# Kernel optimization log

Hardware: AMD Instinct MI355X
Metric: run time of the kernel (lower is better)

The kernel has to match this reference:

```python
import jax, jax.numpy as jnp
import numpy as np

B, TED, G, N, E, MD, NOISE = 10000, 512, 64, 2000, 64000, 15, 128
PAC = 10
PACDIM = (TED + NOISE) * PAC  # 6400
D0, D1 = 1024, 512


def _linear_params(k, fan_in, fan_out):
    kw, kb = jax.random.split(k)
    lim = 1.0 / np.sqrt(fan_in)
    w = jax.random.uniform(kw, (fan_in, fan_out), minval=-lim, maxval=lim, dtype=jnp.float32)
    b = jax.random.uniform(kb, (fan_out,), minval=-lim, maxval=lim, dtype=jnp.float32)
    return w, b


def setup_inputs() -> dict:
    key = jax.random.key(0)
    ks = jax.random.split(key, 12)
    inp = {
        'input_': jax.random.normal(ks[0], (B, TED), dtype=jnp.float32),
        'graphs_x': jax.random.normal(ks[1], (G, N, 1), dtype=jnp.float32),
        'edge_index': jax.random.randint(ks[2], (G, 2, E), 0, N, dtype=jnp.int32),
        'graph_ids': jax.random.randint(ks[3], (B,), 0, G, dtype=jnp.int32),
        'chain': jax.random.normal(ks[4], (B, 1), dtype=jnp.float32),
        'metadata': jax.random.normal(ks[5], (B, MD), dtype=jnp.float32),
    }
    inp['gcn_w'], inp['gcn_b'] = _linear_params(ks[6], 1, 1)
    inp['meta_w'], inp['meta_b'] = _linear_params(ks[7], 1 + MD, 32)
    inp['gme_w'], inp['gme_b'] = _linear_params(ks[8], N + 32, NOISE)
    inp['seq_w0'], inp['seq_b0'] = _linear_params(ks[9], PACDIM, D0)
    inp['seq_w1'], inp['seq_b1'] = _linear_params(ks[10], D0, D1)
    inp['seq_w2'], inp['seq_b2'] = _linear_params(ks[11], D1, 1)
    return inp


def _gcn_one(x, ei, gcn_w, gcn_b):
    # GCNConv(1,1) with self-loops and symmetric normalization.
    loops = jnp.arange(N, dtype=ei.dtype)
    src = jnp.concatenate([ei[0], loops])
    dst = jnp.concatenate([ei[1], loops])
    deg = jax.ops.segment_sum(jnp.ones_like(src, dtype=x.dtype), dst, num_segments=N)
    dinv = jax.lax.rsqrt(deg)  # deg >= 1 due to self-loops
    norm = dinv[src] * dinv[dst]  # [E+N]
    xw = x @ gcn_w  # [N,1]
    msg = xw[src] * norm[:, None]
    out = jax.ops.segment_sum(msg, dst, num_segments=N) + gcn_b
    return out.reshape(-1)  # flatten -> [N]


def reference(input_, graphs_x, edge_index, graph_ids, chain, metadata,
              gcn_w, gcn_b, meta_w, meta_b, gme_w, gme_b,
              seq_w0, seq_b0, seq_w1, seq_b1, seq_w2, seq_b2):
    # per-unique-graph GCN, vectorized over G graphs
    gcn_out = jax.vmap(lambda x, ei: _gcn_one(x, ei, gcn_w, gcn_b))(graphs_x, edge_index)  # [G,N]
    graph_emb = gcn_out[graph_ids]  # gather: [B,N]
    all_meta = jnp.concatenate([chain, metadata], axis=1)  # [B,1+MD]
    meta_emb = jax.nn.relu(all_meta @ meta_w + meta_b)  # [B,32]
    noise = jnp.concatenate([graph_emb, meta_emb], axis=1) @ gme_w + gme_b  # [B,NOISE]
    h = jnp.concatenate([input_, noise], axis=1).reshape(-1, PACDIM)  # [B/PAC, PACDIM]
    h = jax.nn.leaky_relu(h @ seq_w0 + seq_b0, 0.2)  # dropout omitted (eval mode)
    h = jax.nn.leaky_relu(h @ seq_w1 + seq_b1, 0.2)
    return h @ seq_w2 + seq_b2  # [B/PAC, 1]
```

## Files before the change

### kernel.cpp

```cpp
#include <hip/hip_runtime.h>

typedef __bf16 bf16_t;
typedef __bf16 bf16x4 __attribute__((ext_vector_type(4)));
typedef __bf16 bf16x8 __attribute__((ext_vector_type(8)));
typedef float floatx4 __attribute__((ext_vector_type(4)));

#define G_GRAPHS 64
#define N_NODES 2000
#define N_EDGES 64000
#define BATCH 10000
#define TED_ 512
#define NOISE_ 128
#define PACDIM_ 6400
#define D0_ 1024
#define D1_ 512
#define MROWS 1000
#define ESPLIT 8
#define EPB (N_EDGES / ESPLIT)
#define S0 8
#define S1 8

__device__ __forceinline__ void glds16(const void* g, void* l) {
    __builtin_amdgcn_global_load_lds(
        (__attribute__((address_space(1))) void*)(g),
        (__attribute__((address_space(3))) void*)(l), 16, 0, 0);
}

__global__ __launch_bounds__(256) void prep_kernel(
    const int* __restrict__ edge_index, float* __restrict__ degs_part,
    const float* __restrict__ in, bf16_t* __restrict__ A,
    const float* __restrict__ W0, bf16_t* __restrict__ W0t,
    const float* __restrict__ W1, bf16_t* __restrict__ W1t)
{
    __shared__ float h[N_NODES];
    __shared__ float t[32][33];
    const int b = blockIdx.x, tid = threadIdx.x;
    if (b < 512) {
        const int s = b & 7, g = b >> 3;
        for (int n = tid; n < N_NODES; n += 256) h[n] = 0.f;
        __syncthreads();
        const int* dst = edge_index + (size_t)g * 2 * N_EDGES + N_EDGES + s * EPB;
        for (int e = tid; e < EPB; e += 256) atomicAdd(&h[dst[e]], 1.0f);
        __syncthreads();
        float* dp = degs_part + ((size_t)g * ESPLIT + s) * N_NODES;
        for (int n = tid; n < N_NODES; n += 256) dp[n] = h[n];
        return;
    }
    if (b < 5512) {
        int idx = (b - 512) * 256 + tid;
        float4 v = ((const float4*)in)[idx];
        int bb = idx >> 7;
        int c = (idx & 127) << 2;
        int r = bb / 10, slot = bb - r * 10;
        bf16x4 o = { (bf16_t)v.x, (bf16_t)v.y, (bf16_t)v.z, (bf16_t)v.w };
        *(bf16x4*)(A + (size_t)r * PACDIM_ + slot * 640 + c) = o;
        return;
    }
    const float* W; bf16_t* Wt; int Rr, Cc, c0, r0;
    if (b < 11912) {
        int tile = b - 5512;
        W = W0; Wt = W0t; Rr = PACDIM_; Cc = D0_;
        c0 = (tile & 31) << 5; r0 = (tile >> 5) << 5;
    } else {
        int tile = b - 11912;
        W = W1; Wt = W1t; Rr = D0_; Cc = D1_;
        c0 = (tile & 15) << 5; r0 = (tile >> 4) << 5;
    }
    int tx = tid & 31, ty = tid >> 5;
    for (int yy = ty; yy < 32; yy += 8)
        t[yy][tx] = W[(size_t)(r0 + yy) * Cc + c0 + tx];
    __syncthreads();
    for (int yy = ty; yy < 32; yy += 8)
        Wt[(size_t)(c0 + yy) * Rr + r0 + tx] = (bf16_t)t[tx][yy];
}

__global__ __launch_bounds__(512) void msg_kernel(
    const float* __restrict__ graphs_x, const int* __restrict__ edge_index,
    const float* __restrict__ degs_part, float* __restrict__ outs_part)
{
    __shared__ float xs[N_NODES];
    __shared__ float dv[N_NODES];
    __shared__ float oh[N_NODES];
    const int g = blockIdx.y, s = blockIdx.x, tid = threadIdx.x;
    const float* xg = graphs_x + (size_t)g * N_NODES;
    const float* dgp = degs_part + (size_t)g * ESPLIT * N_NODES;
    for (int n = tid; n < N_NODES; n += 512) {
        xs[n] = xg[n];
        float d = 1.0f;
        for (int p = 0; p < ESPLIT; p++) d += dgp[(size_t)p * N_NODES + n];
        dv[n] = rsqrtf(d);
        oh[n] = 0.f;
    }
    __syncthreads();
    const int* src = edge_index + (size_t)g * 2 * N_EDGES + s * EPB;
    const int* dst = src + N_EDGES;
    for (int e = tid; e < EPB; e += 512) {
        int ss = src[e], dd = dst[e];
        atomicAdd(&oh[dd], xs[ss] * dv[ss] * dv[dd]);
    }
    __syncthreads();
    float* op = outs_part + ((size_t)g * ESPLIT + s) * N_NODES;
    for (int n = tid; n < N_NODES; n += 512) op[n] = oh[n];
}

__global__ __launch_bounds__(512) void gnoise_kernel(
    const float* __restrict__ graphs_x, const float* __restrict__ degs_part,
    const float* __restrict__ outs_part,
    const float* __restrict__ gcn_w, const float* __restrict__ gcn_b,
    const float* __restrict__ gme_w, float* __restrict__ gnoise_p)
{
    __shared__ float of[500];
    __shared__ float part[4][128];
    const int s = blockIdx.x, g = blockIdx.y, tid = threadIdx.x;
    const int nBase = s * 500;
    const float w = gcn_w[0], bb = gcn_b[0];
    const float* dgp = degs_part + (size_t)g * ESPLIT * N_NODES;
    const float* otp = outs_part + (size_t)g * ESPLIT * N_NODES;
    for (int n = tid; n < 500; n += 512) {
        int gn = nBase + n;
        float d = 1.0f, o = 0.f;
        for (int p = 0; p < ESPLIT; p++) {
            d += dgp[(size_t)p * N_NODES + gn];
            o += otp[(size_t)p * N_NODES + gn];
        }
        of[n] = w * (o + graphs_x[(size_t)g * N_NODES + gn] / d) + bb;
    }
    __syncthreads();
    const int j = tid & 127, ch = tid >> 7;
    float acc = 0.f;
    const int n0 = ch * 125;
    for (int n = n0; n < n0 + 125; n++)
        acc += of[n] * gme_w[(size_t)(nBase + n) * 128 + j];
    part[ch][j] = acc;
    __syncthreads();
    if (tid < 128)
        gnoise_p[((size_t)g * 4 + s) * 128 + tid] =
            part[0][tid] + part[1][tid] + part[2][tid] + part[3][tid];
}

__global__ __launch_bounds__(256) void meta_kernel(
    const float* __restrict__ chain, const float* __restrict__ metadata,
    const int* __restrict__ graph_ids,
    const float* __restrict__ meta_w, const float* __restrict__ meta_b,
    const float* __restrict__ gme_w, const float* __restrict__ gme_b,
    const float* __restrict__ gnoise_p, bf16_t* __restrict__ A)
{
    int wid = (blockIdx.x * 256 + threadIdx.x) >> 6;
    int lane = threadIdx.x & 63;
    if (wid >= BATCH) return;
    const int b = wid;
    float me = 0.f;
    if (lane < 32) {
        me = meta_b[lane] + chain[b] * meta_w[lane];
        for (int i = 1; i < 16; i++)
            me += metadata[(size_t)b * 15 + (i - 1)] * meta_w[(size_t)i * 32 + lane];
        me = me > 0.f ? me : 0.f;
    }
    const int gid = graph_ids[b];
    const float* gp = gnoise_p + (size_t)gid * 4 * 128;
    const int j1 = lane, j2 = lane + 64;
    float n1 = gme_b[j1] + gp[j1] + gp[128 + j1] + gp[256 + j1] + gp[384 + j1];
    float n2 = gme_b[j2] + gp[j2] + gp[128 + j2] + gp[256 + j2] + gp[384 + j2];
    for (int k = 0; k < 32; k++) {
        float mk = __shfl(me, k, 64);
        const float* wrow = gme_w + (size_t)(N_NODES + k) * 128;
        n1 += mk * wrow[j1];
        n2 += mk * wrow[j2];
    }
    int r = b / 10, slot = b - r * 10;
    bf16_t* dp = A + (size_t)r * PACDIM_ + slot * 640 + TED_;
    dp[j1] = (bf16_t)n1;
    dp[j2] = (bf16_t)n2;
}

__global__ __launch_bounds__(256) void gemm_bt_splitk_kernel(
    const bf16_t* __restrict__ A,
    const bf16_t* __restrict__ Bt,
    float* __restrict__ P,
    int M, int N, int K, int KS, int zbits, int xbits, int Mp)
{
    __shared__ __align__(16) bf16_t As[2][128 * 32];
    __shared__ __align__(16) bf16_t Bs[2][128 * 32];
    const int tid = threadIdx.x;
    const int wave = tid >> 6;
    const int lane = tid & 63;
    const int id = blockIdx.x;
    const int z = id & ((1 << zbits) - 1);
    const int xt = (id >> zbits) & ((1 << xbits) - 1);
    const int yt = id >> (zbits + xbits);
    const int mBase = yt * 128;
    const int nBase = xt * 128;
    const int wm = (wave & 1) * 64;
    const int wn = (wave >> 1) * 64;

    floatx4 acc[4][4] = {};

    const int rA0 = tid >> 2, k80 = (tid & 3) * 8;
    int gm0 = mBase + rA0;      if (gm0 > M - 1) gm0 = M - 1;
    int gm1 = mBase + 64 + rA0; if (gm1 > M - 1) gm1 = M - 1;
    const bf16_t* aP0 = A + (size_t)gm0 * K + k80;
    const bf16_t* aP1 = A + (size_t)gm1 * K + k80;
    const bf16_t* bP0 = Bt + (size_t)(nBase + rA0) * K + k80;
    const bf16_t* bP1 = Bt + (size_t)(nBase + 64 + rA0) * K + k80;

    const int kq = (lane >> 4) * 8;
    const int mr = lane & 15;
    int aOff[4], bOff[4];
    for (int i = 0; i < 4; i++) aOff[i] = (wm + i * 16 + mr) * 32 + kq;
    for (int j = 0; j < 4; j++) bOff[j] = (wn + j * 16 + mr) * 32 + kq;

    const int nIter = KS >> 5;
    const int kc = z * KS;
    {
        char* lA = (char*)(&As[0][0]) + wave * 1024;
        char* lB = (char*)(&Bs[0][0]) + wave * 1024;
        glds16(aP0 + kc, lA);
        glds16(aP1 + kc, lA + 4096);
        glds16(bP0 + kc, lB);
        glds16(bP1 + kc, lB + 4096);
    }
    __syncthreads();
    for (int t = 0; t < nIter; ++t) {
        const int cur = t & 1;
        if (t + 1 < nIter) {
            const int kn = kc + (t + 1) * 32;
            char* lA = (char*)(&As[cur ^ 1][0]) + wave * 1024;
            char* lB = (char*)(&Bs[cur ^ 1][0]) + wave * 1024;
            glds16(aP0 + kn, lA);
            glds16(aP1 + kn, lA + 4096);
            glds16(bP0 + kn, lB);
            glds16(bP1 + kn, lB + 4096);
        }
        const bf16_t* aB = &As[cur][0];
        const bf16_t* bB = &Bs[cur][0];
        bf16x8 af[4], bfr[4];
        for (int i = 0; i < 4; i++) af[i] = *(const bf16x8*)(aB + aOff[i]);
        for (int j = 0; j < 4; j++) bfr[j] = *(const bf16x8*)(bB + bOff[j]);
        for (int i = 0; i < 4; i++)
            for (int j = 0; j < 4; j++)
                acc[i][j] = __builtin_amdgcn_mfma_f32_16x16x32_bf16(
                    af[i], bfr[j], acc[i][j], 0, 0, 0);
        __syncthreads();
    }

    float* Pz = P + (size_t)z * Mp * N;
    const int rq = (lane >> 4) * 4;
    const int cn = lane & 15;
    for (int j = 0; j < 4; j++) {
        int col = nBase + wn + j * 16 + cn;
        for (int i = 0; i < 4; i++)
            for (int r = 0; r < 4; r++) {
                int rowm = mBase + wm + i * 16 + rq + r;
                Pz[(size_t)rowm * N + col] = acc[i][j][r];
            }
    }
}

__global__ __launch_bounds__(256) void reduce_bias_leaky_kernel(
    const float* __restrict__ P, const float* __restrict__ bias,
    bf16_t* __restrict__ C, int M, int N, int Mp, int S)
{
    int idx = blockIdx.x * 256 + threadIdx.x;
    int total = M * (N >> 2);
    if (idx >= total) return;
    int nv = N >> 2;
    int r = idx / nv, c4 = (idx - r * nv) << 2;
    size_t off = (size_t)r * N + c4;
    size_t stride = (size_t)Mp * N;
    float4 v = *(const float4*)(P + off);
    for (int s = 1; s < S; s++) {
        float4 u = *(const float4*)(P + s * stride + off);
        v.x += u.x; v.y += u.y; v.z += u.z; v.w += u.w;
    }
    const float4 bv = *(const float4*)(bias + c4);
    v.x += bv.x; v.y += bv.y; v.z += bv.z; v.w += bv.w;
    v.x = v.x > 0.f ? v.x : 0.2f * v.x;
    v.y = v.y > 0.f ? v.y : 0.2f * v.y;
    v.z = v.z > 0.f ? v.z : 0.2f * v.z;
    v.w = v.w > 0.f ? v.w : 0.2f * v.w;
    bf16x4 o = { (bf16_t)v.x, (bf16_t)v.y, (bf16_t)v.z, (bf16_t)v.w };
    *(bf16x4*)(C + off) = o;
}

__global__ __launch_bounds__(256) void final_fused_kernel(
    const float* __restrict__ P, const float* __restrict__ b1,
    const float* __restrict__ w2, const float* __restrict__ b2,
    float* __restrict__ out, int Mp, int S)
{
    int wid = (blockIdx.x * 256 + threadIdx.x) >> 6;
    int lane = threadIdx.x & 63;
    if (wid >= MROWS) return;
    size_t stride = (size_t)Mp * D1_;
    const float* base = P + (size_t)wid * D1_;
    float s = 0.f;
    for (int i = 0; i < 8; i++) {
        int c = i * 64 + lane;
        float v = base[c];
        for (int z = 1; z < S; z++) v += base[(size_t)z * stride + c];
        v += b1[c];
        v = v > 0.f ? v : 0.2f * v;
        s += v * w2[c];
    }
    for (int off = 32; off; off >>= 1) s += __shfl_down(s, off, 64);
    if (lane == 0) out[wid] = s + b2[0];
}

extern "C" void kernel_launch(void* const* d_in, const int* in_sizes, int n_in,
                              void* d_out, int out_size, void* d_ws, size_t ws_size,
                              hipStream_t stream)
{
    const float* input_    = (const float*)d_in[0];
    const float* graphs_x  = (const float*)d_in[1];
    const int*   edge_idx  = (const int*)  d_in[2];
    const int*   graph_ids = (const int*)  d_in[3];
    const float* chain     = (const float*)d_in[4];
    const float* metadata  = (const float*)d_in[5];
    const float* gcn_w     = (const float*)d_in[6];
    const float* gcn_b     = (const float*)d_in[7];
    const float* meta_w    = (const float*)d_in[8];
    const float* meta_b    = (const float*)d_in[9];
    const float* gme_w     = (const float*)d_in[10];
    const float* gme_b     = (const float*)d_in[11];
    const float* seq_w0    = (const float*)d_in[12];
    const float* seq_b0    = (const float*)d_in[13];
    const float* seq_w1    = (const float*)d_in[14];
    const float* seq_b1    = (const float*)d_in[15];
    const float* seq_w2    = (const float*)d_in[16];
    const float* seq_b2    = (const float*)d_in[17];
    float* out = (float*)d_out;

    char* ws = (char*)d_ws;
    float*  degs_part = (float*)(ws + 0);
    float*  outs_part = (float*)(ws + 4096000);
    float*  gnoise_p  = (float*)(ws + 8192000);
    bf16_t* Abuf      = (bf16_t*)(ws + 8323072);
    bf16_t* W0t       = (bf16_t*)(ws + 21123072);
    bf16_t* W1t       = (bf16_t*)(ws + 34230272);
    bf16_t* H1        = (bf16_t*)(ws + 35278848);
    float*  P         = (float*)(ws + 37326848);

    prep_kernel<<<12424, 256, 0, stream>>>(
        edge_idx, degs_part, input_, Abuf, seq_w0, W0t, seq_w1, W1t);
    msg_kernel<<<dim3(ESPLIT, G_GRAPHS), 512, 0, stream>>>(
        graphs_x, edge_idx, degs_part, outs_part);
    gnoise_kernel<<<dim3(4, G_GRAPHS), 512, 0, stream>>>(
        graphs_x, degs_part, outs_part, gcn_w, gcn_b, gme_w, gnoise_p);
    meta_kernel<<<2500, 256, 0, stream>>>(
        chain, metadata, graph_ids, meta_w, meta_b, gme_w, gme_b,
        gnoise_p, Abuf);

    gemm_bt_splitk_kernel<<<512, 256, 0, stream>>>(
        Abuf, W0t, P, MROWS, D0_, PACDIM_, PACDIM_ / S0, 3, 3, 1024);
    reduce_bias_leaky_kernel<<<(MROWS * D0_ / 4 + 255) / 256, 256, 0, stream>>>(
        P, seq_b0, H1, MROWS, D0_, 1024, S0);

    gemm_bt_splitk_kernel<<<256, 256, 0, stream>>>(
        H1, W1t, P, MROWS, D1_, D0_, D0_ / S1, 3, 2, 1024);
    final_fused_kernel<<<(MROWS * 64 + 255) / 256, 256, 0, stream>>>(
        P, seq_b1, seq_w2, seq_b2, out, 1024, S1);
}
```

Measured before the change: 265.6 us.

## Swizzle GEMM LDS layout, split message pass finer, vectorize edge loads

The GEMM tile loader and fragment reader now XOR-swizzle the 8-element k-groups by row, so LDS reads of the bf16 tiles hit fewer bank conflicts. The GCN message kernel splits edges 16 ways instead of 8 and precomputes x*dinv per node, dropping one multiply and one LDS read per edge. Degree and message edge loops use int4 and int2 vector loads. The workspace layout is shifted to hold the larger partial buffer, and gnoise now sums 16 message partials, which adds a little reduction work.

```diff
diff --git a/kernel.cpp b/kernel.cpp
--- a/kernel.cpp
+++ b/kernel.cpp
@@ -17,6 +17,8 @@
 #define MROWS 1000
 #define ESPLIT 8
 #define EPB (N_EDGES / ESPLIT)
+#define MSPLIT 16
+#define EPB_MSG (N_EDGES / MSPLIT)
 #define S0 8
 #define S1 8
 
@@ -39,8 +41,13 @@
         const int s = b & 7, g = b >> 3;
         for (int n = tid; n < N_NODES; n += 256) h[n] = 0.f;
         __syncthreads();
-        const int* dst = edge_index + (size_t)g * 2 * N_EDGES + N_EDGES + s * EPB;
-        for (int e = tid; e < EPB; e += 256) atomicAdd(&h[dst[e]], 1.0f);
+        const int4* d4 = (const int4*)(edge_index + (size_t)g * 2 * N_EDGES
+                                       + N_EDGES + s * EPB);
+        for (int e = tid; e < EPB / 4; e += 256) {
+            int4 v = d4[e];
+            atomicAdd(&h[v.x], 1.0f); atomicAdd(&h[v.y], 1.0f);
+            atomicAdd(&h[v.z], 1.0f); atomicAdd(&h[v.w], 1.0f);
+        }
         __syncthreads();
         float* dp = degs_part + ((size_t)g * ESPLIT + s) * N_NODES;
         for (int n = tid; n < N_NODES; n += 256) dp[n] = h[n];
@@ -78,28 +85,31 @@
     const float* __restrict__ graphs_x, const int* __restrict__ edge_index,
     const float* __restrict__ degs_part, float* __restrict__ outs_part)
 {
-    __shared__ float xs[N_NODES];
-    __shared__ float dv[N_NODES];
+    __shared__ float ys[N_NODES];
+    __shared__ float dvl[N_NODES];
     __shared__ float oh[N_NODES];
     const int g = blockIdx.y, s = blockIdx.x, tid = threadIdx.x;
     const float* xg = graphs_x + (size_t)g * N_NODES;
     const float* dgp = degs_part + (size_t)g * ESPLIT * N_NODES;
     for (int n = tid; n < N_NODES; n += 512) {
-        xs[n] = xg[n];
         float d = 1.0f;
         for (int p = 0; p < ESPLIT; p++) d += dgp[(size_t)p * N_NODES + n];
-        dv[n] = rsqrtf(d);
+        float dv = rsqrtf(d);
+        dvl[n] = dv;
+        ys[n] = xg[n] * dv;
         oh[n] = 0.f;
     }
     __syncthreads();
-    const int* src = edge_index + (size_t)g * 2 * N_EDGES + s * EPB;
-    const int* dst = src + N_EDGES;
-    for (int e = tid; e < EPB; e += 512) {
-        int ss = src[e], dd = dst[e];
-        atomicAdd(&oh[dd], xs[ss] * dv[ss] * dv[dd]);
-    }
-    __syncthreads();
-    float* op = outs_part + ((size_t)g * ESPLIT + s) * N_NODES;
+    const int* src = edge_index + (size_t)g * 2 * N_EDGES + s * EPB_MSG;
+    const int2* s2 = (const int2*)src;
+    const int2* d2 = (const int2*)(src + N_EDGES);
+    for (int e = tid; e < EPB_MSG / 2; e += 512) {
+        int2 sv = s2[e], dd = d2[e];
+        atomicAdd(&oh[dd.x], ys[sv.x] * dvl[dd.x]);
+        atomicAdd(&oh[dd.y], ys[sv.y] * dvl[dd.y]);
+    }
+    __syncthreads();
+    float* op = outs_part + ((size_t)g * MSPLIT + s) * N_NODES;
     for (int n = tid; n < N_NODES; n += 512) op[n] = oh[n];
 }
 
@@ -115,14 +125,12 @@
     const int nBase = s * 500;
     const float w = gcn_w[0], bb = gcn_b[0];
     const float* dgp = degs_part + (size_t)g * ESPLIT * N_NODES;
-    const float* otp = outs_part + (size_t)g * ESPLIT * N_NODES;
+    const float* otp = outs_part + (size_t)g * MSPLIT * N_NODES;
     for (int n = tid; n < 500; n += 512) {
         int gn = nBase + n;
         float d = 1.0f, o = 0.f;
-        for (int p = 0; p < ESPLIT; p++) {
-            d += dgp[(size_t)p * N_NODES + gn];
-            o += otp[(size_t)p * N_NODES + gn];
-        }
+        for (int p = 0; p < ESPLIT; p++) d += dgp[(size_t)p * N_NODES + gn];
+        for (int p = 0; p < MSPLIT; p++) o += otp[(size_t)p * N_NODES + gn];
         of[n] = w * (o + graphs_x[(size_t)g * N_NODES + gn] / d) + bb;
     }
     __syncthreads();
@@ -195,16 +203,20 @@
 
     floatx4 acc[4][4] = {};
 
-    const int rA0 = tid >> 2, k80 = (tid & 3) * 8;
+    const int rA0 = tid >> 2;
+    const int g4 = tid & 3;
+    const int f4 = (rA0 >> 1) & 3;
+    const int k8 = (g4 ^ f4) * 8;
     int gm0 = mBase + rA0;      if (gm0 > M - 1) gm0 = M - 1;
     int gm1 = mBase + 64 + rA0; if (gm1 > M - 1) gm1 = M - 1;
-    const bf16_t* aP0 = A + (size_t)gm0 * K + k80;
-    const bf16_t* aP1 = A + (size_t)gm1 * K + k80;
-    const bf16_t* bP0 = Bt + (size_t)(nBase + rA0) * K + k80;
-    const bf16_t* bP1 = Bt + (size_t)(nBase + 64 + rA0) * K + k80;
-
-    const int kq = (lane >> 4) * 8;
+    const bf16_t* aP0 = A + (size_t)gm0 * K + k8;
+    const bf16_t* aP1 = A + (size_t)gm1 * K + k8;
+    const bf16_t* bP0 = Bt + (size_t)(nBase + rA0) * K + k8;
+    const bf16_t* bP1 = Bt + (size_t)(nBase + 64 + rA0) * K + k8;
+
+    const int q4 = lane >> 4;
     const int mr = lane & 15;
+    const int kq = ((q4 ^ ((mr >> 1) & 3)) * 8);
     int aOff[4], bOff[4];
     for (int i = 0; i < 4; i++) aOff[i] = (wm + i * 16 + mr) * 32 + kq;
     for (int j = 0; j < 4; j++) bOff[j] = (wn + j * 16 + mr) * 32 + kq;
@@ -332,16 +344,16 @@
     char* ws = (char*)d_ws;
     float*  degs_part = (float*)(ws + 0);
     float*  outs_part = (float*)(ws + 4096000);
-    float*  gnoise_p  = (float*)(ws + 8192000);
-    bf16_t* Abuf      = (bf16_t*)(ws + 8323072);
-    bf16_t* W0t       = (bf16_t*)(ws + 21123072);
-    bf16_t* W1t       = (bf16_t*)(ws + 34230272);
-    bf16_t* H1        = (bf16_t*)(ws + 35278848);
-    float*  P         = (float*)(ws + 37326848);
+    float*  gnoise_p  = (float*)(ws + 12288000);
+    bf16_t* Abuf      = (bf16_t*)(ws + 12419072);
+    bf16_t* W0t       = (bf16_t*)(ws + 25219072);
+    bf16_t* W1t       = (bf16_t*)(ws + 38326272);
+    bf16_t* H1        = (bf16_t*)(ws + 39374848);
+    float*  P         = (float*)(ws + 41422848);
 
     prep_kernel<<<12424, 256, 0, stream>>>(
         edge_idx, degs_part, input_, Abuf, seq_w0, W0t, seq_w1, W1t);
-    msg_kernel<<<dim3(ESPLIT, G_GRAPHS), 512, 0, stream>>>(
+    msg_kernel<<<dim3(MSPLIT, G_GRAPHS), 512, 0, stream>>>(
         graphs_x, edge_idx, degs_part, outs_part);
     gnoise_kernel<<<dim3(4, G_GRAPHS), 512, 0, stream>>>(
         graphs_x, degs_part, outs_part, gcn_w, gcn_b, gme_w, gnoise_p);
```

New measurement: 264.2 us. No clear change (-0.5%).
